# Optimization experiments

Measured on AMD Instinct MI355X. Metric: run time of the kernel, lower is better.

Reference implementation:

```python
import jax, jax.numpy as jnp
import numpy as np

B, C = 4096, 1024  # batch_size, label_size (== embedding_dim of dense outputs)


def setup_inputs() -> dict:
    key = jax.random.key(0)
    k1, k2, k3 = jax.random.split(key, 3)
    return {
        "outs": jax.random.normal(k1, (B, C), dtype=jnp.float32),
        "class_centers": jax.random.normal(k2, (C, C), dtype=jnp.float32),
        "batch_label": jax.random.randint(k3, (B,), 0, C, dtype=jnp.int32),
    }


def reference(outs, class_centers, batch_label):
    b, c = outs.shape
    # ---- standard cross-entropy (F.cross_entropy, mean reduction) ----
    logp = jax.nn.log_softmax(outs, axis=-1)
    ce = -jnp.mean(jnp.take_along_axis(logp, batch_label[:, None].astype(jnp.int32), axis=1))

    # ---- InfoNCE with Wasserstein hard-negative mining ----
    # memory bank stores detached embeddings -> centers carry no gradient
    centers = jax.lax.stop_gradient(class_centers)
    pos = centers[batch_label]  # [B, C] positive per anchor

    # calculate_2_wasserstein_dist on 1-D vectors reduces EXACTLY to
    # ||x - y||^2 - 2*d*sqrt(1e-15)  (covariance terms vanish for a single column)
    const = jnp.float32(-2.0 * c * np.sqrt(1e-15))
    x = jax.lax.stop_gradient(outs)  # similarity used only for index selection
    sq = jnp.sum(x * x, axis=-1)  # [B]
    sim = sq[:, None] + sq[None, :] - 2.0 * (x @ x.T) + const  # [B, B]

    # negatives: different label (self automatically excluded: same label)
    mask = batch_label[:, None] != batch_label[None, :]  # [B, B]
    neg_inf = jnp.float32(-1e30)
    # hard negative: largest wasserstein distance among negatives (topk k=1)
    hard_idx = jnp.argmax(jnp.where(mask, sim, neg_inf), axis=1)  # [B]
    # random negative: uniform over negatives via Gumbel-max (torch randperm analogue)
    g = jax.random.gumbel(jax.random.key(42), (b, b), dtype=jnp.float32)
    rand_idx = jnp.argmax(jnp.where(mask, g, neg_inf), axis=1)  # [B]

    pos_sim = jnp.sum(outs * pos, axis=-1)                # [B]
    n_rand = jnp.sum(outs * outs[rand_idx], axis=-1)      # [B]
    n_hard = jnp.sum(outs * outs[hard_idx], axis=-1)      # [B]
    logits = jnp.stack([pos_sim, n_rand, n_hard], axis=1)  # [B, 1+num_negatives]
    info_nce = -jnp.mean(jax.nn.log_softmax(logits, axis=1)[:, 0])

    return ce + 0.1 * info_nce
```

## Files before the change

kernel.cpp:

```cpp
#include <hip/hip_runtime.h>
#include <hip/hip_bf16.h>
#include <stdint.h>

#define Bsz 4096
#define Csz 1024

typedef __attribute__((ext_vector_type(8))) short short8;
typedef __attribute__((ext_vector_type(4))) float f32x4;

__device__ __forceinline__ unsigned fenc(float v) {
  unsigned u = __float_as_uint(v);
  return (u & 0x80000000u) ? ~u : (u | 0x80000000u);
}

__device__ __forceinline__ void load_lds16(const void* g, void* l) {
  __builtin_amdgcn_global_load_lds(
      (const __attribute__((address_space(1))) void*)g,
      (__attribute__((address_space(3))) void*)l, 16, 0, 0);
}

__device__ __forceinline__ uint32_t rotl32(uint32_t x, int r) {
  return (x << r) | (x >> (32 - r));
}

__global__ __launch_bounds__(256) void k_rowstats(
    const float* __restrict__ outs, const int* __restrict__ label,
    unsigned short* __restrict__ xb, float* __restrict__ sq,
    float* __restrict__ ce, unsigned long long* __restrict__ hard) {
  const int row = blockIdx.x;
  const int tid = threadIdx.x;
  const int lane = tid & 63, wid = tid >> 6;
  const float4 v = reinterpret_cast<const float4*>(outs + (size_t)row * Csz)[tid];

  ushort4 u4;
  {
    __hip_bfloat16 h;
    h = __float2bfloat16(v.x); u4.x = *reinterpret_cast<const unsigned short*>(&h);
    h = __float2bfloat16(v.y); u4.y = *reinterpret_cast<const unsigned short*>(&h);
    h = __float2bfloat16(v.z); u4.z = *reinterpret_cast<const unsigned short*>(&h);
    h = __float2bfloat16(v.w); u4.w = *reinterpret_cast<const unsigned short*>(&h);
  }
  reinterpret_cast<ushort4*>(xb + (size_t)row * Csz)[tid] = u4;

  __shared__ float wred[3][4];
  float mx = fmaxf(fmaxf(v.x, v.y), fmaxf(v.z, v.w));
#pragma unroll
  for (int off = 32; off; off >>= 1) mx = fmaxf(mx, __shfl_xor(mx, off, 64));
  if (lane == 0) wred[0][wid] = mx;
  __syncthreads();
  mx = fmaxf(fmaxf(wred[0][0], wred[0][1]), fmaxf(wred[0][2], wred[0][3]));

  float se = expf(v.x - mx) + expf(v.y - mx) + expf(v.z - mx) + expf(v.w - mx);
  float s2 = v.x * v.x + v.y * v.y + v.z * v.z + v.w * v.w;
#pragma unroll
  for (int off = 32; off; off >>= 1) {
    se += __shfl_xor(se, off, 64);
    s2 += __shfl_xor(s2, off, 64);
  }
  if (lane == 0) { wred[1][wid] = se; wred[2][wid] = s2; }
  __syncthreads();
  if (tid == 0) {
    const float set = wred[1][0] + wred[1][1] + wred[1][2] + wred[1][3];
    const float sqt = wred[2][0] + wred[2][1] + wred[2][2] + wred[2][3];
    sq[row] = sqt;
    ce[row] = -(outs[(size_t)row * Csz + label[row]] - mx - logf(set));
    hard[row] = 0ull;
  }
}

__global__ __launch_bounds__(256) void k_hard(
    const unsigned short* __restrict__ xb, const float* __restrict__ sq,
    const int* __restrict__ label, unsigned long long* __restrict__ hard) {
  __shared__ unsigned short As[2][128 * 64];
  __shared__ unsigned short Bs[2][128 * 64];

  int rem = blockIdx.x, bi = 0;
  while (rem >= 32 - bi) { rem -= 32 - bi; ++bi; }
  const int bj = bi + rem;

  const int tid = threadIdx.x;
  const int wid = tid >> 6, lane = tid & 63;
  const int wr = wid >> 1, wc = wid & 1;
  const int fr = lane & 15;
  const int fq = lane >> 4;
  const int sx = lane & 7;

  f32x4 acc[4][4];
#pragma unroll
  for (int m = 0; m < 4; ++m)
#pragma unroll
    for (int n = 0; n < 4; ++n) acc[m][n] = (f32x4){0.f, 0.f, 0.f, 0.f};

  const unsigned short* Ag = xb + (size_t)(bi * 128) * Csz;
  const unsigned short* Bg = xb + (size_t)(bj * 128) * Csz;
  const int lrow = lane >> 3;
  const int lch = ((lane & 7) ^ lrow) * 8;

  auto STAGE = [&](int buf, int kt) {
#pragma unroll
    for (int c = 0; c < 4; ++c) {
      const int r = wid * 32 + c * 8;
      load_lds16(Ag + (size_t)(r + lrow) * Csz + kt + lch, &As[buf][r * 64]);
      load_lds16(Bg + (size_t)(r + lrow) * Csz + kt + lch, &Bs[buf][r * 64]);
    }
  };
  auto COMPUTE = [&](int buf) {
#pragma unroll
    for (int ks = 0; ks < 2; ++ks) {
      const int choff = ((ks * 4 + fq) ^ sx) * 8;
      short8 a[4], b[4];
#pragma unroll
      for (int m = 0; m < 4; ++m)
        a[m] = *reinterpret_cast<const short8*>(
            &As[buf][(wr * 64 + m * 16 + fr) * 64 + choff]);
#pragma unroll
      for (int n = 0; n < 4; ++n)
        b[n] = *reinterpret_cast<const short8*>(
            &Bs[buf][(wc * 64 + n * 16 + fr) * 64 + choff]);
#pragma unroll
      for (int m = 0; m < 4; ++m)
#pragma unroll
        for (int n = 0; n < 4; ++n)
          acc[m][n] = __builtin_amdgcn_mfma_f32_16x16x32_bf16(a[m], b[n], acc[m][n], 0, 0, 0);
    }
  };

  STAGE(0, 0);
  __syncthreads();
  int cur = 0;
  for (int kt = 64; kt < Csz; kt += 64) {
    STAGE(cur ^ 1, kt);
    COMPUTE(cur);
    __syncthreads();
    cur ^= 1;
  }
  COMPUTE(cur);

  const float cst = -2.0f * 1024.0f * 3.1622776601683794e-8f;

#pragma unroll
  for (int m = 0; m < 4; ++m) {
#pragma unroll
    for (int r = 0; r < 4; ++r) {
      const int i = bi * 128 + wr * 64 + m * 16 + fq * 4 + r;
      const int li = label[i];
      const float sqi = sq[i];
      float bestv = -3.0e38f;
      int bestj = 0x7FFFFFFF;
#pragma unroll
      for (int n = 0; n < 4; ++n) {
        const int j = bj * 128 + wc * 64 + n * 16 + fr;
        const float val = sqi + sq[j] - 2.0f * acc[m][n][r] + cst;
        if (label[j] != li && val > bestv) { bestv = val; bestj = j; }
      }
      unsigned long long pack =
          (bestj == 0x7FFFFFFF)
              ? 0ull
              : (((unsigned long long)fenc(bestv)) << 32) | (unsigned)(~bestj);
#pragma unroll
      for (int off = 1; off < 16; off <<= 1) {
        unsigned long long o = __shfl_xor(pack, off, 64);
        if (o > pack) pack = o;
      }
      if (fr == 0 && pack) atomicMax(&hard[i], pack);
    }
  }

  if (bi != bj) {
#pragma unroll
    for (int n = 0; n < 4; ++n) {
      const int j = bj * 128 + wc * 64 + n * 16 + fr;
      const int lj = label[j];
      const float sqj = sq[j];
      unsigned long long pack = 0ull;
#pragma unroll
      for (int m = 0; m < 4; ++m) {
#pragma unroll
        for (int r = 0; r < 4; ++r) {
          const int i = bi * 128 + wr * 64 + m * 16 + fq * 4 + r;
          if (label[i] != lj) {
            const float val = sq[i] + sqj - 2.0f * acc[m][n][r] + cst;
            const unsigned long long p =
                (((unsigned long long)fenc(val)) << 32) | (unsigned)(~i);
            if (p > pack) pack = p;
          }
        }
      }
      unsigned long long o;
      o = __shfl_xor(pack, 16, 64); if (o > pack) pack = o;
      o = __shfl_xor(pack, 32, 64); if (o > pack) pack = o;
      if (fq == 0 && pack) atomicMax(&hard[j], pack);
    }
  }
}

__global__ __launch_bounds__(256) void k_rand(
    const int* __restrict__ label, int* __restrict__ ridx) {
  const int i = blockIdx.x;
  const int tid = threadIdx.x;
  const int lane = tid & 63, wid = tid >> 6;
  const int li0 = label[i], li1 = label[i + 2048];
  const uint32_t k1c = 42u, k2c = 0x1BD11BDAu ^ 42u;
  unsigned long long b0 = 0ull, b1 = 0ull;
  for (int j = tid; j < Bsz; j += 256) {
    uint32_t x0 = (uint32_t)(i * Bsz + j);
    uint32_t x1 = x0 + 8388608u;
    x1 += k1c;
#define RND(rt) { x0 += x1; x1 = rotl32(x1, rt); x1 ^= x0; }
    RND(13) RND(15) RND(26) RND(6)
    x0 += k1c; x1 += k2c + 1u;
    RND(17) RND(29) RND(16) RND(24)
    x0 += k2c; x1 += 2u;
    RND(13) RND(15) RND(26) RND(6)
    x1 += k1c + 3u;
    RND(17) RND(29) RND(16) RND(24)
    x0 += k1c; x1 += k2c + 4u;
    RND(13) RND(15) RND(26) RND(6)
    x0 += k2c; x1 += 5u;
#undef RND
    const int lj = label[j];
    if (lj != li0) {
      unsigned long long p = (((unsigned long long)(x0 >> 9)) << 32) | (uint32_t)(~j);
      if (p > b0) b0 = p;
    }
    if (lj != li1) {
      unsigned long long p = (((unsigned long long)(x1 >> 9)) << 32) | (uint32_t)(~j);
      if (p > b1) b1 = p;
    }
  }
#pragma unroll
  for (int off = 32; off; off >>= 1) {
    unsigned long long o0 = __shfl_xor(b0, off, 64); if (o0 > b0) b0 = o0;
    unsigned long long o1 = __shfl_xor(b1, off, 64); if (o1 > b1) b1 = o1;
  }
  __shared__ unsigned long long r0[4], r1[4];
  if (lane == 0) { r0[wid] = b0; r1[wid] = b1; }
  __syncthreads();
  if (tid == 0) {
#pragma unroll
    for (int w = 1; w < 4; ++w) {
      if (r0[w] > b0) b0 = r0[w];
      if (r1[w] > b1) b1 = r1[w];
    }
    ridx[i] = (int)(~(uint32_t)b0);
    ridx[i + 2048] = (int)(~(uint32_t)b1);
  }
}

__global__ __launch_bounds__(256) void k_nce(
    const float* __restrict__ outs, const float* __restrict__ centers,
    const int* __restrict__ label, const unsigned long long* __restrict__ hard,
    const int* __restrict__ ridx, float* __restrict__ nce) {
  const int i = blockIdx.x;
  const int tid = threadIdx.x;
  const int lane = tid & 63, wid = tid >> 6;
  const int li = label[i];
  const int jh = (int)(~(uint32_t)hard[i]);
  const int jr = ridx[i];
  const float4 a  = reinterpret_cast<const float4*>(outs + (size_t)i * Csz)[tid];
  const float4 c  = reinterpret_cast<const float4*>(centers + (size_t)li * Csz)[tid];
  const float4 rr = reinterpret_cast<const float4*>(outs + (size_t)jr * Csz)[tid];
  const float4 hh = reinterpret_cast<const float4*>(outs + (size_t)jh * Csz)[tid];
  float dp = a.x * c.x + a.y * c.y + a.z * c.z + a.w * c.w;
  float dr = a.x * rr.x + a.y * rr.y + a.z * rr.z + a.w * rr.w;
  float dh = a.x * hh.x + a.y * hh.y + a.z * hh.z + a.w * hh.w;
#pragma unroll
  for (int off = 32; off; off >>= 1) {
    dp += __shfl_xor(dp, off, 64);
    dr += __shfl_xor(dr, off, 64);
    dh += __shfl_xor(dh, off, 64);
  }
  __shared__ float w0[4], w1[4], w2[4];
  if (lane == 0) { w0[wid] = dp; w1[wid] = dr; w2[wid] = dh; }
  __syncthreads();
  if (tid == 0) {
    const float l0 = w0[0] + w0[1] + w0[2] + w0[3];
    const float l1 = w1[0] + w1[1] + w1[2] + w1[3];
    const float l2 = w2[0] + w2[1] + w2[2] + w2[3];
    const float m = fmaxf(l0, fmaxf(l1, l2));
    const float lse = logf(expf(l0 - m) + expf(l1 - m) + expf(l2 - m));
    nce[i] = -(l0 - m - lse);
  }
}

__global__ __launch_bounds__(1024) void k_final(
    const float* __restrict__ ce, const float* __restrict__ nce,
    float* __restrict__ out) {
  __shared__ double s[1024];
  const int tid = threadIdx.x;
  double v = 0.0;
#pragma unroll
  for (int q = 0; q < 4; ++q) {
    v += (double)ce[tid + q * 1024];
    v += 0.1 * (double)nce[tid + q * 1024];
  }
  s[tid] = v;
  __syncthreads();
  for (int off = 512; off; off >>= 1) {
    if (tid < off) s[tid] += s[tid + off];
    __syncthreads();
  }
  if (tid == 0) out[0] = (float)(s[0] / 4096.0);
}

extern "C" void kernel_launch(void* const* d_in, const int* in_sizes, int n_in,
                              void* d_out, int out_size, void* d_ws, size_t ws_size,
                              hipStream_t stream) {
  const float* outs = (const float*)d_in[0];
  const float* centers = (const float*)d_in[1];
  const int* label = (const int*)d_in[2];
  float* out = (float*)d_out;

  char* ws = (char*)d_ws;
  unsigned short* xb = (unsigned short*)ws;
  unsigned long long* hard = (unsigned long long*)(ws + (8u << 20));
  float* sq = (float*)(ws + (8u << 20) + 32768);
  float* ce = sq + Bsz;
  float* nce = ce + Bsz;
  int* ridx = (int*)(nce + Bsz);

  k_rowstats<<<Bsz, 256, 0, stream>>>(outs, label, xb, sq, ce, hard);
  k_hard<<<528, 256, 0, stream>>>(xb, sq, label, hard);
  k_rand<<<Bsz / 2, 256, 0, stream>>>(label, ridx);
  k_nce<<<Bsz, 256, 0, stream>>>(outs, centers, label, hard, ridx, nce);
  k_final<<<1, 1024, 0, stream>>>(ce, nce, out);
}
```

Before: 169.2 us.

## Fuse random-negative kernel into rowstats and pipeline the hard-negative GEMM

Folds the Gumbel random-negative search into the row-statistics kernel (first 2048 blocks), which removes one kernel launch. The hard-negative GEMM is reworked: blocks are remapped across the upper-triangular tiles with a swizzle, the launch bound allows 2 blocks per CU, and the loads use a two-stage prefetch with explicit vmcnt waits and raw s_barrier instead of __syncthreads. MFMA sections are also raised in priority with s_setprio. The hand-placed waitcnt and barriers give up compiler safety, and the fused rowstats blocks now do much more work, so their load is uneven.

```diff
diff --git a/kernel.cpp b/kernel.cpp
--- a/kernel.cpp
+++ b/kernel.cpp
@@ -26,7 +26,8 @@
 __global__ __launch_bounds__(256) void k_rowstats(
     const float* __restrict__ outs, const int* __restrict__ label,
     unsigned short* __restrict__ xb, float* __restrict__ sq,
-    float* __restrict__ ce, unsigned long long* __restrict__ hard) {
+    float* __restrict__ ce, unsigned long long* __restrict__ hard,
+    int* __restrict__ ridx) {
   const int row = blockIdx.x;
   const int tid = threadIdx.x;
   const int lane = tid & 63, wid = tid >> 6;
@@ -66,139 +67,10 @@
     ce[row] = -(outs[(size_t)row * Csz + label[row]] - mx - logf(set));
     hard[row] = 0ull;
   }
-}
-
-__global__ __launch_bounds__(256) void k_hard(
-    const unsigned short* __restrict__ xb, const float* __restrict__ sq,
-    const int* __restrict__ label, unsigned long long* __restrict__ hard) {
-  __shared__ unsigned short As[2][128 * 64];
-  __shared__ unsigned short Bs[2][128 * 64];
-
-  int rem = blockIdx.x, bi = 0;
-  while (rem >= 32 - bi) { rem -= 32 - bi; ++bi; }
-  const int bj = bi + rem;
-
-  const int tid = threadIdx.x;
-  const int wid = tid >> 6, lane = tid & 63;
-  const int wr = wid >> 1, wc = wid & 1;
-  const int fr = lane & 15;
-  const int fq = lane >> 4;
-  const int sx = lane & 7;
-
-  f32x4 acc[4][4];
-#pragma unroll
-  for (int m = 0; m < 4; ++m)
-#pragma unroll
-    for (int n = 0; n < 4; ++n) acc[m][n] = (f32x4){0.f, 0.f, 0.f, 0.f};
-
-  const unsigned short* Ag = xb + (size_t)(bi * 128) * Csz;
-  const unsigned short* Bg = xb + (size_t)(bj * 128) * Csz;
-  const int lrow = lane >> 3;
-  const int lch = ((lane & 7) ^ lrow) * 8;
-
-  auto STAGE = [&](int buf, int kt) {
-#pragma unroll
-    for (int c = 0; c < 4; ++c) {
-      const int r = wid * 32 + c * 8;
-      load_lds16(Ag + (size_t)(r + lrow) * Csz + kt + lch, &As[buf][r * 64]);
-      load_lds16(Bg + (size_t)(r + lrow) * Csz + kt + lch, &Bs[buf][r * 64]);
-    }
-  };
-  auto COMPUTE = [&](int buf) {
-#pragma unroll
-    for (int ks = 0; ks < 2; ++ks) {
-      const int choff = ((ks * 4 + fq) ^ sx) * 8;
-      short8 a[4], b[4];
-#pragma unroll
-      for (int m = 0; m < 4; ++m)
-        a[m] = *reinterpret_cast<const short8*>(
-            &As[buf][(wr * 64 + m * 16 + fr) * 64 + choff]);
-#pragma unroll
-      for (int n = 0; n < 4; ++n)
-        b[n] = *reinterpret_cast<const short8*>(
-            &Bs[buf][(wc * 64 + n * 16 + fr) * 64 + choff]);
-#pragma unroll
-      for (int m = 0; m < 4; ++m)
-#pragma unroll
-        for (int n = 0; n < 4; ++n)
-          acc[m][n] = __builtin_amdgcn_mfma_f32_16x16x32_bf16(a[m], b[n], acc[m][n], 0, 0, 0);
-    }
-  };
-
-  STAGE(0, 0);
-  __syncthreads();
-  int cur = 0;
-  for (int kt = 64; kt < Csz; kt += 64) {
-    STAGE(cur ^ 1, kt);
-    COMPUTE(cur);
-    __syncthreads();
-    cur ^= 1;
-  }
-  COMPUTE(cur);
-
-  const float cst = -2.0f * 1024.0f * 3.1622776601683794e-8f;
-
-#pragma unroll
-  for (int m = 0; m < 4; ++m) {
-#pragma unroll
-    for (int r = 0; r < 4; ++r) {
-      const int i = bi * 128 + wr * 64 + m * 16 + fq * 4 + r;
-      const int li = label[i];
-      const float sqi = sq[i];
-      float bestv = -3.0e38f;
-      int bestj = 0x7FFFFFFF;
-#pragma unroll
-      for (int n = 0; n < 4; ++n) {
-        const int j = bj * 128 + wc * 64 + n * 16 + fr;
-        const float val = sqi + sq[j] - 2.0f * acc[m][n][r] + cst;
-        if (label[j] != li && val > bestv) { bestv = val; bestj = j; }
-      }
-      unsigned long long pack =
-          (bestj == 0x7FFFFFFF)
-              ? 0ull
-              : (((unsigned long long)fenc(bestv)) << 32) | (unsigned)(~bestj);
-#pragma unroll
-      for (int off = 1; off < 16; off <<= 1) {
-        unsigned long long o = __shfl_xor(pack, off, 64);
-        if (o > pack) pack = o;
-      }
-      if (fr == 0 && pack) atomicMax(&hard[i], pack);
-    }
-  }
-
-  if (bi != bj) {
-#pragma unroll
-    for (int n = 0; n < 4; ++n) {
-      const int j = bj * 128 + wc * 64 + n * 16 + fr;
-      const int lj = label[j];
-      const float sqj = sq[j];
-      unsigned long long pack = 0ull;
-#pragma unroll
-      for (int m = 0; m < 4; ++m) {
-#pragma unroll
-        for (int r = 0; r < 4; ++r) {
-          const int i = bi * 128 + wr * 64 + m * 16 + fq * 4 + r;
-          if (label[i] != lj) {
-            const float val = sq[i] + sqj - 2.0f * acc[m][n][r] + cst;
-            const unsigned long long p =
-                (((unsigned long long)fenc(val)) << 32) | (unsigned)(~i);
-            if (p > pack) pack = p;
-          }
-        }
-      }
-      unsigned long long o;
-      o = __shfl_xor(pack, 16, 64); if (o > pack) pack = o;
-      o = __shfl_xor(pack, 32, 64); if (o > pack) pack = o;
-      if (fq == 0 && pack) atomicMax(&hard[j], pack);
-    }
-  }
-}
-
-__global__ __launch_bounds__(256) void k_rand(
-    const int* __restrict__ label, int* __restrict__ ridx) {
-  const int i = blockIdx.x;
-  const int tid = threadIdx.x;
-  const int lane = tid & 63, wid = tid >> 6;
+
+  if (row >= 2048) return;
+
+  const int i = row;
   const int li0 = label[i], li1 = label[i + 2048];
   const uint32_t k1c = 42u, k2c = 0x1BD11BDAu ^ 42u;
   unsigned long long b0 = 0ull, b1 = 0ull;
@@ -247,6 +119,147 @@
   }
 }
 
+__global__ __launch_bounds__(256, 2) void k_hard(
+    const unsigned short* __restrict__ xb, const float* __restrict__ sq,
+    const int* __restrict__ label, unsigned long long* __restrict__ hard) {
+  __shared__ unsigned short As[2][128 * 64];
+  __shared__ unsigned short Bs[2][128 * 64];
+
+  const int bid = (int)blockIdx.x;
+  const int swz = (bid & 7) * 66 + (bid >> 3);
+  int rem = swz, bi = 0;
+  while (rem >= 32 - bi) { rem -= 32 - bi; ++bi; }
+  const int bj = bi + rem;
+
+  const int tid = (int)threadIdx.x;
+  const int wid = tid >> 6, lane = tid & 63;
+  const int wr = wid >> 1, wc = wid & 1;
+  const int fr = lane & 15;
+  const int fq = lane >> 4;
+  const int sx = fr & 7;
+
+  f32x4 acc[4][4];
+#pragma unroll
+  for (int m = 0; m < 4; ++m)
+#pragma unroll
+    for (int n = 0; n < 4; ++n) acc[m][n] = (f32x4){0.f, 0.f, 0.f, 0.f};
+
+  const unsigned short* Ag = xb + (size_t)(bi * 128) * Csz;
+  const unsigned short* Bg = xb + (size_t)(bj * 128) * Csz;
+  const int lrow = lane >> 3;
+  const int lch = ((lane & 7) ^ lrow) * 8;
+
+  auto STAGE = [&](int buf, int kt) {
+#pragma unroll
+    for (int c = 0; c < 4; ++c) {
+      const int r = wid * 32 + c * 8;
+      load_lds16(Ag + (size_t)(r + lrow) * Csz + kt + lch, &As[buf][r * 64]);
+      load_lds16(Bg + (size_t)(r + lrow) * Csz + kt + lch, &Bs[buf][r * 64]);
+    }
+  };
+  auto COMPUTE = [&](int buf) {
+#pragma unroll
+    for (int ks = 0; ks < 2; ++ks) {
+      const int choff = ((ks * 4 + fq) ^ sx) * 8;
+      short8 a[4], b[4];
+#pragma unroll
+      for (int m = 0; m < 4; ++m)
+        a[m] = *reinterpret_cast<const short8*>(
+            &As[buf][(wr * 64 + m * 16 + fr) * 64 + choff]);
+#pragma unroll
+      for (int n = 0; n < 4; ++n)
+        b[n] = *reinterpret_cast<const short8*>(
+            &Bs[buf][(wc * 64 + n * 16 + fr) * 64 + choff]);
+      __builtin_amdgcn_s_setprio(1);
+#pragma unroll
+      for (int m = 0; m < 4; ++m)
+#pragma unroll
+        for (int n = 0; n < 4; ++n)
+          acc[m][n] = __builtin_amdgcn_mfma_f32_16x16x32_bf16(a[m], b[n], acc[m][n], 0, 0, 0);
+      __builtin_amdgcn_s_setprio(0);
+    }
+  };
+
+  STAGE(0, 0);
+  STAGE(1, 64);
+#pragma unroll 1
+  for (int t = 0; t < 14; ++t) {
+    asm volatile("s_waitcnt vmcnt(8)" ::: "memory");
+    __builtin_amdgcn_sched_barrier(0);
+    __builtin_amdgcn_s_barrier();
+    COMPUTE(t & 1);
+    asm volatile("s_waitcnt lgkmcnt(0)" ::: "memory");
+    __builtin_amdgcn_sched_barrier(0);
+    __builtin_amdgcn_s_barrier();
+    STAGE(t & 1, (t + 2) * 64);
+  }
+  asm volatile("s_waitcnt vmcnt(8)" ::: "memory");
+  __builtin_amdgcn_sched_barrier(0);
+  __builtin_amdgcn_s_barrier();
+  COMPUTE(0);
+  asm volatile("s_waitcnt vmcnt(0)" ::: "memory");
+  __builtin_amdgcn_sched_barrier(0);
+  __builtin_amdgcn_s_barrier();
+  COMPUTE(1);
+
+  const float cst = -2.0f * 1024.0f * 3.1622776601683794e-8f;
+
+#pragma unroll
+  for (int m = 0; m < 4; ++m) {
+#pragma unroll
+    for (int r = 0; r < 4; ++r) {
+      const int i = bi * 128 + wr * 64 + m * 16 + fq * 4 + r;
+      const int li = label[i];
+      const float sqi = sq[i];
+      float bestv = -3.0e38f;
+      int bestj = 0x7FFFFFFF;
+#pragma unroll
+      for (int n = 0; n < 4; ++n) {
+        const int j = bj * 128 + wc * 64 + n * 16 + fr;
+        const float val = sqi + sq[j] - 2.0f * acc[m][n][r] + cst;
+        if (label[j] != li && val > bestv) { bestv = val; bestj = j; }
+      }
+      unsigned long long pack =
+          (bestj == 0x7FFFFFFF)
+              ? 0ull
+              : (((unsigned long long)fenc(bestv)) << 32) | (unsigned)(~bestj);
+#pragma unroll
+      for (int off = 1; off < 16; off <<= 1) {
+        unsigned long long o = __shfl_xor(pack, off, 64);
+        if (o > pack) pack = o;
+      }
+      if (fr == 0 && pack) atomicMax(&hard[i], pack);
+    }
+  }
+
+  if (bi != bj) {
+#pragma unroll
+    for (int n = 0; n < 4; ++n) {
+      const int j = bj * 128 + wc * 64 + n * 16 + fr;
+      const int lj = label[j];
+      const float sqj = sq[j];
+      unsigned long long pack = 0ull;
+#pragma unroll
+      for (int m = 0; m < 4; ++m) {
+#pragma unroll
+        for (int r = 0; r < 4; ++r) {
+          const int i = bi * 128 + wr * 64 + m * 16 + fq * 4 + r;
+          if (label[i] != lj) {
+            const float val = sq[i] + sqj - 2.0f * acc[m][n][r] + cst;
+            const unsigned long long p =
+                (((unsigned long long)fenc(val)) << 32) | (unsigned)(~i);
+            if (p > pack) pack = p;
+          }
+        }
+      }
+      unsigned long long o;
+      o = __shfl_xor(pack, 16, 64); if (o > pack) pack = o;
+      o = __shfl_xor(pack, 32, 64); if (o > pack) pack = o;
+      if (fq == 0 && pack) atomicMax(&hard[j], pack);
+    }
+  }
+}
+
 __global__ __launch_bounds__(256) void k_nce(
     const float* __restrict__ outs, const float* __restrict__ centers,
     const int* __restrict__ label, const unsigned long long* __restrict__ hard,
@@ -319,9 +332,8 @@
   float* nce = ce + Bsz;
   int* ridx = (int*)(nce + Bsz);
 
-  k_rowstats<<<Bsz, 256, 0, stream>>>(outs, label, xb, sq, ce, hard);
+  k_rowstats<<<Bsz, 256, 0, stream>>>(outs, label, xb, sq, ce, hard, ridx);
   k_hard<<<528, 256, 0, stream>>>(xb, sq, label, hard);
-  k_rand<<<Bsz / 2, 256, 0, stream>>>(label, ridx);
   k_nce<<<Bsz, 256, 0, stream>>>(outs, centers, label, hard, ridx, nce);
   k_final<<<1, 1024, 0, stream>>>(ce, nce, out);
 }
```

New measurement: 161.3 us. 1.05x faster.
